# Kernel optimization log

Hardware: AMD Instinct MI355X
Metric: run time of the kernel (lower is better)

The kernel has to match this reference:

```python
import jax, jax.numpy as jnp
import numpy as np
from jax import lax

EPS = 1e-5

def _sign(x):
    # sign with sign(0)=+1, as used in XNOR-style binarization
    return jnp.where(x >= 0, 1.0, -1.0).astype(x.dtype)

def binarize(x):
    # straight-through estimator: forward = sign(x), backward = identity
    return x + lax.stop_gradient(_sign(x) - x)

def batchnorm(x, p):
    # p: [4, C] rows = (gamma, beta, running_mean, running_var); eval-mode BN
    g, b, m, v = p[0], p[1], p[2], p[3]
    shape = (1, -1) + (1,) * (x.ndim - 2)
    inv = g / jnp.sqrt(v + EPS)
    return (x - m.reshape(shape)) * inv.reshape(shape) + b.reshape(shape)

def conv2d(x, w):
    return lax.conv_general_dilated(x, w, window_strides=(1, 1), padding='VALID',
                                    dimension_numbers=('NCHW', 'OIHW', 'NCHW'))

def maxpool2(x):
    return lax.reduce_window(x, -jnp.inf, lax.max, (1, 1, 2, 2), (1, 1, 2, 2), 'VALID')

def hardtanh(x):
    return jnp.clip(x, -1.0, 1.0)


def setup_inputs() -> dict:
    key = jax.random.key(0)
    ks = jax.random.split(key, 16)
    B = 16384
    x = jax.random.normal(ks[0], (B, 3, 22, 22), jnp.float32)
    w1 = jax.random.normal(ks[1], (32, 3, 3, 3), jnp.float32) * 0.1
    w2 = jax.random.normal(ks[2], (32, 32, 3, 3), jnp.float32) * 0.1
    w3 = jax.random.normal(ks[3], (64, 32, 3, 3), jnp.float32) * 0.1
    w_fc1 = jax.random.normal(ks[4], (128, 64), jnp.float32) * 0.1
    w_fc2 = jax.random.normal(ks[5], (2, 128), jnp.float32) * 0.1
    w_fc3 = jax.random.normal(ks[6], (4, 128), jnp.float32) * 0.1

    def make_bn(k, c):
        k1, k2, k3, k4 = jax.random.split(k, 4)
        gamma = jax.random.uniform(k1, (c,), jnp.float32, 0.5, 1.5)
        beta = jax.random.normal(k2, (c,), jnp.float32) * 0.1
        mean = jax.random.normal(k3, (c,), jnp.float32) * 0.1
        var = jax.random.uniform(k4, (c,), jnp.float32, 0.5, 1.5)
        return jnp.stack([gamma, beta, mean, var])  # [4, C]

    bn1 = make_bn(ks[7], 32)
    bn2 = make_bn(ks[8], 32)
    bn3 = make_bn(ks[9], 64)
    bn4 = make_bn(ks[10], 128)
    bn5 = make_bn(ks[11], 2)
    bn6 = make_bn(ks[12], 4)
    return {'x': x, 'w1': w1, 'w2': w2, 'w3': w3, 'w_fc1': w_fc1, 'w_fc2': w_fc2,
            'w_fc3': w_fc3, 'bn1': bn1, 'bn2': bn2, 'bn3': bn3, 'bn4': bn4,
            'bn5': bn5, 'bn6': bn6}


def reference(x, w1, w2, w3, w_fc1, w_fc2, w_fc3, bn1, bn2, bn3, bn4, bn5, bn6):
    # binary=True, binarize_input=True, bitwidth=input_bitwidth=1:
    # every BinarizeConv2d/BinarizeLinear binarizes both its input and weights.
    h = hardtanh(batchnorm(conv2d(binarize(x), binarize(w1)), bn1))   # [B,32,20,20]
    h = maxpool2(h)                                                    # [B,32,10,10]
    h = hardtanh(batchnorm(conv2d(binarize(h), binarize(w2)), bn2))   # [B,32,8,8]
    h = maxpool2(h)                                                    # [B,32,4,4]
    h = hardtanh(batchnorm(conv2d(binarize(h), binarize(w3)), bn3))   # [B,64,2,2]
    h = maxpool2(h)                                                    # [B,64,1,1]
    h = h.reshape(-1, 64)                                              # [B,64]
    h = hardtanh(batchnorm(binarize(h) @ binarize(w_fc1).T, bn4))      # [B,128]
    out1 = jax.nn.softmax(batchnorm(h @ w_fc2.T, bn5), axis=1)         # [B,2]
    out2 = batchnorm(h @ w_fc3.T, bn6)                                 # [B,4]
    return (out1, out2)
```

## Files before the change

### kernel.cpp

```cpp
#include <hip/hip_runtime.h>
#include <cstdint>
#include <cmath>

#define OFF_W1   0
#define OFF_T1   32
#define OFF_W2   64
#define OFF_T2   352
#define OFF_W3   384
#define OFF_T3   960
#define OFF_WFC1 1024
#define OFF_A4   1280
#define OFF_C4   1408
#define OFF_WF2  1536
#define OFF_WF3  1792
#define OFF_BN5  2304
#define OFF_BN6  2308

__device__ __forceinline__ int thr_neg(double nterms, double g, double b, double m, double v) {
    double inv = g / sqrt(v + 1e-5);
    double t = m - b / inv;
    double thr = floor((nterms - t) * 0.5);
    if (thr < -2147000000.0) thr = -2147000000.0;
    if (thr >  2147000000.0) thr =  2147000000.0;
    return -((int)thr + 1);
}

__global__ void k_prep(const float* __restrict__ w1, const float* __restrict__ w2,
                       const float* __restrict__ w3, const float* __restrict__ wfc1,
                       const float* __restrict__ wfc2, const float* __restrict__ wfc3,
                       const float* __restrict__ bn1, const float* __restrict__ bn2,
                       const float* __restrict__ bn3, const float* __restrict__ bn4,
                       const float* __restrict__ bn5, const float* __restrict__ bn6,
                       unsigned int* __restrict__ ws) {
    __shared__ float stage[9216];
    int t = threadIdx.x;
    int blk = blockIdx.x;
    float* wsf = (float*)ws;
    int*   wsi = (int*)ws;

    if (blk == 0) {
        for (int i = t; i < 864; i += 256) stage[i] = w1[i];
        __syncthreads();
        if (t < 32) {
            unsigned int bits = 0;
            for (int j = 0; j < 27; ++j) bits |= (stage[t*27+j] >= 0.f ? 1u : 0u) << j;
            ws[OFF_W1 + t] = bits;
            wsi[OFF_T1 + t] = thr_neg(27.0,  bn1[t], bn1[32+t], bn1[64+t], bn1[96+t]);
            wsi[OFF_T2 + t] = thr_neg(288.0, bn2[t], bn2[32+t], bn2[64+t], bn2[96+t]);
        }
        for (int i = t; i < 256; i += 256) wsf[OFF_WF2 + i] = wfc2[i];
        for (int i = t; i < 512; i += 256) wsf[OFF_WF3 + i] = wfc3[i];
        if (t < 2) {
            float g = bn5[t], b = bn5[2+t], m = bn5[4+t], v = bn5[6+t];
            float inv = g / sqrtf(v + 1e-5f);
            wsf[OFF_BN5 + t]     = inv;
            wsf[OFF_BN5 + 2 + t] = b - m * inv;
        }
        if (t >= 4 && t < 8) {
            int j = t - 4;
            float g = bn6[j], b = bn6[4+j], m = bn6[8+j], v = bn6[12+j];
            float inv = g / sqrtf(v + 1e-5f);
            wsf[OFF_BN6 + j]     = inv;
            wsf[OFF_BN6 + 4 + j] = b - m * inv;
        }
    } else if (blk == 1) {
        for (int i = t; i < 9216; i += 256) stage[i] = w2[i];
        __syncthreads();
        for (int idx = t; idx < 288; idx += 256) {
            int o = idx / 9, k = idx - o*9;
            unsigned int bits = 0;
            for (int i = 0; i < 32; ++i)
                bits |= (stage[(o*32+i)*9 + k] >= 0.f ? 1u : 0u) << i;
            ws[OFF_W2 + idx] = bits;
        }
    } else if (blk == 2 || blk == 3) {
        int base = (blk - 2) * 9216;
        for (int i = t; i < 9216; i += 256) stage[i] = w3[base + i];
        __syncthreads();
        for (int idx = t; idx < 288; idx += 256) {
            int o = idx / 9, k = idx - o*9;
            unsigned int bits = 0;
            for (int i = 0; i < 32; ++i)
                bits |= (stage[(o*32+i)*9 + k] >= 0.f ? 1u : 0u) << i;
            ws[OFF_W3 + base/32 + idx] = bits;
        }
    } else {
        for (int i = t; i < 8192; i += 256) stage[i] = wfc1[i];
        __syncthreads();
        if (t < 128) {
            unsigned int lo = 0, hi = 0;
            for (int j = 0; j < 32; ++j) lo |= (stage[t*64+j]    >= 0.f ? 1u : 0u) << j;
            for (int j = 0; j < 32; ++j) hi |= (stage[t*64+32+j] >= 0.f ? 1u : 0u) << j;
            ws[OFF_WFC1 + 2*t]     = lo;
            ws[OFF_WFC1 + 2*t + 1] = hi;
            float g = bn4[t], b = bn4[128+t], m = bn4[256+t], v = bn4[384+t];
            float inv = g / sqrtf(v + 1e-5f);
            wsf[OFF_A4 + t] = -2.f * inv;
            wsf[OFF_C4 + t] = (64.f - m) * inv + b;
        }
        if (t >= 128 && t < 192) {
            int j = t - 128;
            wsi[OFF_T3 + j] = thr_neg(288.0, bn3[j], bn3[64+j], bn3[128+j], bn3[192+j]);
        }
    }
}

#define WSTRIDE 584
__global__ __launch_bounds__(256) void k_main(const float* __restrict__ x,
                                              const unsigned int* __restrict__ ws,
                                              float* __restrict__ out, int B) {
    __shared__ unsigned int s_u[4 * WSTRIDE];

    const int tid = threadIdx.x & 63;
    const int wid = threadIdx.x >> 6;
    const int b   = blockIdx.x * 4 + wid;
    if (b >= B) return;
    const float* wsf = (const float*)ws;
    const int*   wsi = (const int*)ws;

    unsigned int* inrow = s_u + wid * WSTRIDE;
    unsigned int* c1    = inrow + 66;
    unsigned int* pb1   = c1 + 400;
    unsigned int* pb2   = pb1 + 100;

    for (int r = tid; r < 66; r += 64) {
        int c = r / 22, y = r - c*22;
        const float2* p = (const float2*)(x + ((size_t)b*3 + c)*484 + (size_t)y*22);
        unsigned int bits = 0;
        #pragma unroll
        for (int j = 0; j < 11; ++j) {
            float2 v = p[j];
            bits |= (v.x >= 0.f ? 1u : 0u) << (2*j);
            bits |= (v.y >= 0.f ? 1u : 0u) << (2*j+1);
        }
        inrow[r] = bits;
    }
    __builtin_amdgcn_wave_barrier();

    for (int pos = tid; pos < 400; pos += 64) {
        int y = pos / 20, xx = pos - y*20;
        unsigned int g = 0;
        #pragma unroll
        for (int c = 0; c < 3; ++c)
            #pragma unroll
            for (int dy = 0; dy < 3; ++dy)
                g |= ((inrow[c*22 + y + dy] >> xx) & 7u) << (c*9 + dy*3);
        unsigned int word = 0;
        #pragma unroll
        for (int o = 31; o >= 0; --o) {
            unsigned int s = (unsigned int)(__popc(g ^ ws[OFF_W1 + o]) + wsi[OFF_T1 + o]);
            word = __builtin_amdgcn_alignbit(word, s, 31);
        }
        c1[pos] = word;
    }
    __builtin_amdgcn_wave_barrier();

    for (int p = tid; p < 100; p += 64) {
        int py = p / 10, px = p - py*10;
        int base = (2*py)*20 + 2*px;
        pb1[p] = c1[base] | c1[base+1] | c1[base+20] | c1[base+21];
    }
    __builtin_amdgcn_wave_barrier();

    {
        int y = tid >> 3, xx = tid & 7;
        unsigned int in9[9];
        #pragma unroll
        for (int dy = 0; dy < 3; ++dy)
            #pragma unroll
            for (int dx = 0; dx < 3; ++dx)
                in9[dy*3+dx] = pb1[(y+dy)*10 + xx + dx];
        unsigned int word = 0;
        #pragma unroll
        for (int o = 31; o >= 0; --o) {
            int s = wsi[OFF_T2 + o];
            #pragma unroll
            for (int k = 0; k < 9; ++k)
                s += __popc(in9[k] ^ ws[OFF_W2 + o*9 + k]);
            word = __builtin_amdgcn_alignbit(word, (unsigned int)s, 31);
        }
        word |= __shfl_xor(word, 1);
        word |= __shfl_xor(word, 8);
        if ((tid & 9) == 0)
            pb2[(y>>1)*4 + (xx>>1)] = word;
    }
    __builtin_amdgcn_wave_barrier();

    unsigned long long b3 = 0;
    {
        unsigned int bb[16];
        #pragma unroll
        for (int i = 0; i < 16; ++i) bb[i] = pb2[i];
        unsigned int w3r[9];
        #pragma unroll
        for (int k = 0; k < 9; ++k) w3r[k] = ws[OFF_W3 + tid*9 + k];
        int negt = wsi[OFF_T3 + tid];
        unsigned int oracc = 0;
        #pragma unroll
        for (int py = 0; py < 2; ++py)
            #pragma unroll
            for (int px = 0; px < 2; ++px) {
                int s = negt;
                #pragma unroll
                for (int dy = 0; dy < 3; ++dy)
                    #pragma unroll
                    for (int dx = 0; dx < 3; ++dx)
                        s += __popc(bb[(py+dy)*4 + px + dx] ^ w3r[dy*3+dx]);
                oracc |= (unsigned int)s;
            }
        b3 = __ballot((int)oracc < 0);
    }

    float h0, h1;
    {
        const unsigned long long* wfc1b = (const unsigned long long*)(ws + OFF_WFC1);
        int pc0 = __popcll(b3 ^ wfc1b[tid]);
        int pc1 = __popcll(b3 ^ wfc1b[tid + 64]);
        float p0 = fmaf((float)pc0, wsf[OFF_A4 + tid],      wsf[OFF_C4 + tid]);
        float p1 = fmaf((float)pc1, wsf[OFF_A4 + tid + 64], wsf[OFF_C4 + tid + 64]);
        h0 = fminf(1.f, fmaxf(-1.f, p0));
        h1 = fminf(1.f, fmaxf(-1.f, p1));
    }

    {
        float part[6];
        #pragma unroll
        for (int j = 0; j < 2; ++j)
            part[j] = h0 * wsf[OFF_WF2 + j*128 + tid] + h1 * wsf[OFF_WF2 + j*128 + 64 + tid];
        #pragma unroll
        for (int j = 0; j < 4; ++j)
            part[2+j] = h0 * wsf[OFF_WF3 + j*128 + tid] + h1 * wsf[OFF_WF3 + j*128 + 64 + tid];
        #pragma unroll
        for (int off = 32; off; off >>= 1) {
            #pragma unroll
            for (int j = 0; j < 6; ++j)
                part[j] += __shfl_xor(part[j], off);
        }
        if (tid < 6) {
            if (tid < 2) {
                float y0 = part[0]*wsf[OFF_BN5+0] + wsf[OFF_BN5+2];
                float y1 = part[1]*wsf[OFF_BN5+1] + wsf[OFF_BN5+3];
                float mx = fmaxf(y0, y1);
                float e0 = expf(y0 - mx), e1 = expf(y1 - mx);
                float r  = 1.f / (e0 + e1);
                out[(size_t)b*2 + tid] = (tid == 0 ? e0 : e1) * r;
            } else {
                int j = tid - 2;
                out[(size_t)B*2 + (size_t)b*4 + j] = part[2+j]*wsf[OFF_BN6+j] + wsf[OFF_BN6+4+j];
            }
        }
    }
}

extern "C" void kernel_launch(void* const* d_in, const int* in_sizes, int n_in,
                              void* d_out, int out_size, void* d_ws, size_t ws_size,
                              hipStream_t stream) {
    const float* x    = (const float*)d_in[0];
    const float* w1   = (const float*)d_in[1];
    const float* w2   = (const float*)d_in[2];
    const float* w3   = (const float*)d_in[3];
    const float* wfc1 = (const float*)d_in[4];
    const float* wfc2 = (const float*)d_in[5];
    const float* wfc3 = (const float*)d_in[6];
    const float* bn1  = (const float*)d_in[7];
    const float* bn2  = (const float*)d_in[8];
    const float* bn3  = (const float*)d_in[9];
    const float* bn4  = (const float*)d_in[10];
    const float* bn5  = (const float*)d_in[11];
    const float* bn6  = (const float*)d_in[12];
    unsigned int* ws  = (unsigned int*)d_ws;
    float* out        = (float*)d_out;
    int B = in_sizes[0] / 1452;

    k_prep<<<5, 256, 0, stream>>>(w1, w2, w3, wfc1, wfc2, wfc3,
                                  bn1, bn2, bn3, bn4, bn5, bn6, ws);
    k_main<<<(B + 3) / 4, 256, 0, stream>>>(x, ws, out, B);
}
```

Measured before the change: 191.0 us.

## Compute binary conv2 with int8 MFMA instead of XOR-popcount

Expands pooled binary activations into ±1 int8 bytes in shared memory and pre-packs conv2 weights as ±1 int8 MFMA B-fragments. Conv2 is then done as nine 32x32x32 int8 MFMA steps per tile, with the accumulators seeded by a negated ceil-threshold, and the maxpool is done through accumulator max plus ballot. This replaces 288 popcounts per lane with matrix-core work, at the cost of extra shared memory per wave, a byte-expansion pass, and a different layout for the bit words written to pb2.

Measured after the change: 184.3 us. 3.5% less time.

```diff
diff --git a/kernel.cpp b/kernel.cpp
--- a/kernel.cpp
+++ b/kernel.cpp
@@ -2,10 +2,12 @@
 #include <cstdint>
 #include <cmath>
 
+typedef int  v4i  __attribute__((ext_vector_type(4)));
+typedef int  v16i __attribute__((ext_vector_type(16)));
+typedef unsigned int u32x4 __attribute__((ext_vector_type(4)));
+
 #define OFF_W1   0
 #define OFF_T1   32
-#define OFF_W2   64
-#define OFF_T2   352
 #define OFF_W3   384
 #define OFF_T3   960
 #define OFF_WFC1 1024
@@ -15,6 +17,8 @@
 #define OFF_WF3  1792
 #define OFF_BN5  2304
 #define OFF_BN6  2308
+#define OFF_B2   2560
+#define OFF_T2C  4864
 
 __device__ __forceinline__ int thr_neg(double nterms, double g, double b, double m, double v) {
     double inv = g / sqrt(v + 1e-5);
@@ -23,6 +27,15 @@
     if (thr < -2147000000.0) thr = -2147000000.0;
     if (thr >  2147000000.0) thr =  2147000000.0;
     return -((int)thr + 1);
+}
+
+__device__ __forceinline__ int thr_c_neg(double g, double b, double m, double v) {
+    double inv = g / sqrt(v + 1e-5);
+    double t = m - b / inv;
+    double ct = ceil(t);
+    if (ct < -2147000000.0) ct = -2147000000.0;
+    if (ct >  2147000000.0) ct =  2147000000.0;
+    return -(int)ct;
 }
 
 __global__ void k_prep(const float* __restrict__ w1, const float* __restrict__ w2,
@@ -45,8 +58,8 @@
             unsigned int bits = 0;
             for (int j = 0; j < 27; ++j) bits |= (stage[t*27+j] >= 0.f ? 1u : 0u) << j;
             ws[OFF_W1 + t] = bits;
-            wsi[OFF_T1 + t] = thr_neg(27.0,  bn1[t], bn1[32+t], bn1[64+t], bn1[96+t]);
-            wsi[OFF_T2 + t] = thr_neg(288.0, bn2[t], bn2[32+t], bn2[64+t], bn2[96+t]);
+            wsi[OFF_T1 + t]  = thr_neg(27.0, bn1[t], bn1[32+t], bn1[64+t], bn1[96+t]);
+            wsi[OFF_T2C + t] = thr_c_neg(bn2[t], bn2[32+t], bn2[64+t], bn2[96+t]);
         }
         for (int i = t; i < 256; i += 256) wsf[OFF_WF2 + i] = wfc2[i];
         for (int i = t; i < 512; i += 256) wsf[OFF_WF3 + i] = wfc3[i];
@@ -66,12 +79,21 @@
     } else if (blk == 1) {
         for (int i = t; i < 9216; i += 256) stage[i] = w2[i];
         __syncthreads();
-        for (int idx = t; idx < 288; idx += 256) {
-            int o = idx / 9, k = idx - o*9;
-            unsigned int bits = 0;
-            for (int i = 0; i < 32; ++i)
-                bits |= (stage[(o*32+i)*9 + k] >= 0.f ? 1u : 0u) << i;
-            ws[OFF_W2 + idx] = bits;
+        for (int idx = t; idx < 2304; idx += 256) {
+            int s   = idx >> 8;
+            int rem = idx & 255;
+            int l   = rem >> 2;
+            int reg = rem & 3;
+            int och = l & 31;
+            int icb = ((l >> 5) << 4) + (reg << 2);
+            unsigned int wv = 0;
+            #pragma unroll
+            for (int j = 0; j < 4; ++j) {
+                int ic = icb + j;
+                unsigned int by = (stage[(och*32 + ic)*9 + s] >= 0.f) ? 0x01u : 0xFFu;
+                wv |= by << (8*j);
+            }
+            ws[OFF_B2 + idx] = wv;
         }
     } else if (blk == 2 || blk == 3) {
         int base = (blk - 2) * 9216;
@@ -105,11 +127,11 @@
     }
 }
 
-#define WSTRIDE 584
+#define WSTRIDE 916
 __global__ __launch_bounds__(256) void k_main(const float* __restrict__ x,
                                               const unsigned int* __restrict__ ws,
                                               float* __restrict__ out, int B) {
-    __shared__ unsigned int s_u[4 * WSTRIDE];
+    __shared__ __align__(16) unsigned int s_u[4 * WSTRIDE];
 
     const int tid = threadIdx.x & 63;
     const int wid = threadIdx.x >> 6;
@@ -118,10 +140,11 @@
     const float* wsf = (const float*)ws;
     const int*   wsi = (const int*)ws;
 
-    unsigned int* inrow = s_u + wid * WSTRIDE;
-    unsigned int* c1    = inrow + 66;
-    unsigned int* pb1   = c1 + 400;
-    unsigned int* pb2   = pb1 + 100;
+    unsigned int* bytes = s_u + wid * WSTRIDE;
+    unsigned int* inrow = bytes;
+    unsigned int* c1    = bytes + 66;
+    unsigned int* pb1   = bytes + 800;
+    unsigned int* pb2   = bytes + 900;
 
     for (int r = tid; r < 66; r += 64) {
         int c = r / 22, y = r - c*22;
@@ -162,27 +185,57 @@
     }
     __builtin_amdgcn_wave_barrier();
 
+    #pragma unroll
+    for (int i = 0; i < 4; ++i) {
+        int ch = tid + 64*i;
+        if (ch < 200) {
+            unsigned int w = pb1[ch >> 1];
+            int sh = (ch & 1) << 4;
+            u32x4 o;
+            #pragma unroll
+            for (int j = 0; j < 4; ++j) {
+                unsigned int nib = (w >> (sh + 4*j)) & 0xFu;
+                unsigned int sp  = (nib * 0x204081u) & 0x01010101u;
+                o[j] = __builtin_amdgcn_perm(0u, 0x000001FFu, sp);
+            }
+            *(u32x4*)(bytes + ch*4) = o;
+        }
+    }
+    __builtin_amdgcn_wave_barrier();
+
     {
-        int y = tid >> 3, xx = tid & 7;
-        unsigned int in9[9];
-        #pragma unroll
-        for (int dy = 0; dy < 3; ++dy)
-            #pragma unroll
-            for (int dx = 0; dx < 3; ++dx)
-                in9[dy*3+dx] = pb1[(y+dy)*10 + xx + dx];
-        unsigned int word = 0;
-        #pragma unroll
-        for (int o = 31; o >= 0; --o) {
-            int s = wsi[OFF_T2 + o];
-            #pragma unroll
-            for (int k = 0; k < 9; ++k)
-                s += __popc(in9[k] ^ ws[OFF_W2 + o*9 + k]);
-            word = __builtin_amdgcn_alignbit(word, (unsigned int)s, 31);
-        }
-        word |= __shfl_xor(word, 1);
-        word |= __shfl_xor(word, 8);
-        if ((tid & 9) == 0)
-            pb2[(y>>1)*4 + (xx>>1)] = word;
+        int nthr2 = wsi[OFF_T2C + (tid & 31)];
+        const v4i* __restrict__ Bfr = (const v4i*)(ws + OFF_B2);
+        #pragma unroll
+        for (int tile = 0; tile < 2; ++tile) {
+            int r   = tid & 31;
+            int gq  = tile*8 + (r >> 2);
+            int sub = r & 3;
+            int y   = ((gq >> 2) << 1) + (sub >> 1);
+            int x   = ((gq & 3) << 1) + (sub & 1);
+            const v4i* __restrict__ Ab = (const v4i*)(bytes + (y*10 + x)*8 + ((tid >> 5) << 2));
+            v16i acc;
+            #pragma unroll
+            for (int j = 0; j < 16; ++j) acc[j] = nthr2;
+            #pragma unroll
+            for (int s = 0; s < 9; ++s) {
+                int dy = s / 3, dx = s - dy*3;
+                v4i a  = Ab[(dy*10 + dx)*2];
+                v4i bf = Bfr[s*64 + tid];
+                acc = __builtin_amdgcn_mfma_i32_32x32x32_i8(a, bf, acc, 0, 0, 0);
+            }
+            #pragma unroll
+            for (int g = 0; g < 4; ++g) {
+                int m0 = acc[4*g]   > acc[4*g+1] ? acc[4*g]   : acc[4*g+1];
+                int m1 = acc[4*g+2] > acc[4*g+3] ? acc[4*g+2] : acc[4*g+3];
+                int mx = m0 > m1 ? m0 : m1;
+                unsigned long long bal = __ballot(mx >= 0);
+                if (tid == 0) {
+                    pb2[tile*8 + 2*g]     = (unsigned int)bal;
+                    pb2[tile*8 + 2*g + 1] = (unsigned int)(bal >> 32);
+                }
+            }
+        }
     }
     __builtin_amdgcn_wave_barrier();
 
```
